# Kernel optimization log

Hardware: AMD Instinct MI355X
Metric: run time of the kernel (lower is better)

The kernel has to match this reference:

```python
import jax, jax.numpy as jnp
import numpy as np

D_H = 128
BATCH = 131072


def setup_inputs() -> dict:
    key = jax.random.key(0)
    k_h, k_x, k_w = jax.random.split(key, 3)
    h = jax.random.normal(k_h, (BATCH, D_H), dtype=jnp.float32)
    x = jax.random.normal(k_x, (BATCH, 3 * D_H), dtype=jnp.float32)
    # Dense kernel (d_h, 3*d_h); original uses zeros init, but random weights
    # give a meaningful correctness baseline.
    W = jax.random.normal(k_w, (D_H, 3 * D_H), dtype=jnp.float32) * 0.05
    return {"h": h, "x": x, "W": W}


def reference(h, x, W):
    d_h = h.shape[-1]
    # recurrent_proj(h): (B, d_h) @ (d_h, 3*d_h) -> (B, 3*d_h)
    recurrent_t = jnp.einsum("bd,de->be", h, W)
    # input pre-activation uses first d_h slice; gates use remaining 2*d_h
    input_t = jnp.tanh(x[:, :d_h] + recurrent_t[:, :d_h])
    gates_t = jax.nn.sigmoid(x[:, d_h:] + recurrent_t[:, d_h:])
    input_gate_t, output_gate_t = jnp.split(gates_t, 2, axis=-1)
    forget_gate_t = 1.0 - input_gate_t  # tied gates
    h_new = input_t * input_gate_t + h * forget_gate_t
    y = jnp.tanh(h_new) * output_gate_t
    return (h_new, y)
```

## Files before the change

### kernel.cpp

```cpp
#include <hip/hip_runtime.h>
#include <hip/hip_bf16.h>

#define BATCH 131072
#define DH 128
#define D3 384

typedef float   f32x4  __attribute__((ext_vector_type(4)));
typedef __bf16  bf16x8 __attribute__((ext_vector_type(8)));
typedef unsigned short u16x8 __attribute__((ext_vector_type(8)));

__device__ __forceinline__ unsigned short f2bf(float f) {
    unsigned u = __builtin_bit_cast(unsigned, f);
    u += 0x7fffu + ((u >> 16) & 1u);
    return (unsigned short)(u >> 16);
}

__device__ __forceinline__ float fast_tanh(float v) {
    float e = __expf(2.0f * v);
    return (e - 1.0f) * __builtin_amdgcn_rcpf(e + 1.0f);
}
__device__ __forceinline__ float fast_sigmoid(float z) {
    return __builtin_amdgcn_rcpf(1.0f + __expf(-z));
}

__global__ void prep_kernel(const float* __restrict__ W, unsigned short* __restrict__ wt) {
    int i   = blockIdx.x * 256 + threadIdx.x;
    int col = i >> 7;
    int k   = i & 127;
    wt[i] = f2bf(W[k * D3 + col]);
}

__global__ __launch_bounds__(256) void fused_kernel(
    const float* __restrict__ h, const float* __restrict__ x,
    const unsigned short* __restrict__ wt, float* __restrict__ out)
{
    const int wave = (blockIdx.x * 256 + (int)threadIdx.x) >> 6;
    const int lane = threadIdx.x & 63;
    const int c    = lane & 15;
    const int g    = lane >> 4;
    const int R    = wave * 16;

    bf16x8 a[4];
    {
        const float* hrow = h + (size_t)(R + c) * DH;
        #pragma unroll
        for (int s = 0; s < 4; ++s) {
            const float4* p = reinterpret_cast<const float4*>(hrow + 32 * s + 8 * g);
            float4 u0 = p[0], u1 = p[1];
            u16x8 t;
            t[0]=f2bf(u0.x); t[1]=f2bf(u0.y); t[2]=f2bf(u0.z); t[3]=f2bf(u0.w);
            t[4]=f2bf(u1.x); t[5]=f2bf(u1.y); t[6]=f2bf(u1.z); t[7]=f2bf(u1.w);
            a[s] = __builtin_bit_cast(bf16x8, t);
        }
    }

    f32x4 acc[24];
    #pragma unroll
    for (int i = 0; i < 24; ++i) acc[i] = (f32x4){0.f, 0.f, 0.f, 0.f};

    #pragma unroll
    for (int n = 0; n < 24; ++n) {
        const u16x8* wp = reinterpret_cast<const u16x8*>(wt + (16 * n + c) * DH);
        #pragma unroll
        for (int s = 0; s < 4; ++s) {
            u16x8 bv = wp[4 * s + g];
            acc[n] = __builtin_amdgcn_mfma_f32_16x16x32_bf16(
                a[s], __builtin_bit_cast(bf16x8, bv), acc[n], 0, 0, 0);
        }
    }

    const size_t ybase = (size_t)BATCH * DH;
    #pragma unroll
    for (int j = 0; j < 4; ++j) {
        const int row = R + 4 * g + j;
        const float* xr = x + (size_t)row * D3;
        const float* hr = h + (size_t)row * DH;
        float* o0 = out + (size_t)row * DH;
        float* o1 = out + ybase + (size_t)row * DH;
        #pragma unroll
        for (int n = 0; n < 8; ++n) {
            const int d = 16 * n + c;
            float r0 = acc[n][j];
            float r1 = acc[8 + n][j];
            float r2 = acc[16 + n][j];
            float hv = hr[d];
            float it = fast_tanh(xr[d] + r0);
            float ig = fast_sigmoid(xr[DH + d] + r1);
            float og = fast_sigmoid(xr[2 * DH + d] + r2);
            float hn = it * ig + hv * (1.0f - ig);
            o0[d] = hn;
            o1[d] = fast_tanh(hn) * og;
        }
    }
}

extern "C" void kernel_launch(void* const* d_in, const int* in_sizes, int n_in,
                              void* d_out, int out_size, void* d_ws, size_t ws_size,
                              hipStream_t stream) {
    const float* h = (const float*)d_in[0];
    const float* x = (const float*)d_in[1];
    const float* W = (const float*)d_in[2];
    float* out = (float*)d_out;
    unsigned short* wt = (unsigned short*)d_ws;

    prep_kernel<<<192, 256, 0, stream>>>(W, wt);
    fused_kernel<<<BATCH / 16 / 4, 256, 0, stream>>>(h, x, wt, out);
}
```

Baseline: 409.7 us.

## Transpose MFMA operands so accumulators hold contiguous row elements, vectorize epilogue I/O

Swaps the MFMA operand roles (W as A, h as B) so each lane's accumulator holds 4 contiguous output columns of one row. This allows x to be preloaded into the accumulators with 16-byte nontemporal loads and outputs to be written with 16-byte nontemporal stores, replacing the scalar strided epilogue accesses. Work is split so two waves share a 16-row tile, each covering half the columns, which doubles the grid and cuts accumulator registers from 24 to 12 vectors. In exchange, h is loaded and converted twice per tile, and the prep kernel's write pattern changes.

```diff
diff --git a/kernel.cpp b/kernel.cpp
--- a/kernel.cpp
+++ b/kernel.cpp
@@ -14,7 +14,6 @@
     u += 0x7fffu + ((u >> 16) & 1u);
     return (unsigned short)(u >> 16);
 }
-
 __device__ __forceinline__ float fast_tanh(float v) {
     float e = __expf(2.0f * v);
     return (e - 1.0f) * __builtin_amdgcn_rcpf(e + 1.0f);
@@ -24,10 +23,9 @@
 }
 
 __global__ void prep_kernel(const float* __restrict__ W, unsigned short* __restrict__ wt) {
-    int i   = blockIdx.x * 256 + threadIdx.x;
-    int col = i >> 7;
-    int k   = i & 127;
-    wt[i] = f2bf(W[k * D3 + col]);
+    const int k = blockIdx.x;
+    const int e = threadIdx.x;
+    wt[e * DH + k] = f2bf(W[k * D3 + e]);
 }
 
 __global__ __launch_bounds__(256) void fused_kernel(
@@ -38,59 +36,67 @@
     const int lane = threadIdx.x & 63;
     const int c    = lane & 15;
     const int g    = lane >> 4;
-    const int R    = wave * 16;
+    const int tile = wave >> 1;
+    const int q    = wave & 1;
+    const int row  = tile * 16 + c;
+    const int dbase = 64 * q + 4 * g;
 
-    bf16x8 a[4];
-    {
-        const float* hrow = h + (size_t)(R + c) * DH;
+    const float* xr = x + (size_t)row * D3;
+    const float* hr = h + (size_t)row * DH;
+
+    f32x4 acc[3][4];
+    #pragma unroll
+    for (int grp = 0; grp < 3; ++grp) {
         #pragma unroll
-        for (int s = 0; s < 4; ++s) {
-            const float4* p = reinterpret_cast<const float4*>(hrow + 32 * s + 8 * g);
-            float4 u0 = p[0], u1 = p[1];
-            u16x8 t;
-            t[0]=f2bf(u0.x); t[1]=f2bf(u0.y); t[2]=f2bf(u0.z); t[3]=f2bf(u0.w);
-            t[4]=f2bf(u1.x); t[5]=f2bf(u1.y); t[6]=f2bf(u1.z); t[7]=f2bf(u1.w);
-            a[s] = __builtin_bit_cast(bf16x8, t);
+        for (int n = 0; n < 4; ++n) {
+            const f32x4* p = reinterpret_cast<const f32x4*>(xr + grp * DH + dbase + 16 * n);
+            acc[grp][n] = __builtin_nontemporal_load(p);
         }
     }
 
-    f32x4 acc[24];
+    bf16x8 b[4];
     #pragma unroll
-    for (int i = 0; i < 24; ++i) acc[i] = (f32x4){0.f, 0.f, 0.f, 0.f};
+    for (int s = 0; s < 4; ++s) {
+        const float4* p = reinterpret_cast<const float4*>(hr + 32 * s + 8 * g);
+        float4 u0 = p[0], u1 = p[1];
+        u16x8 t;
+        t[0]=f2bf(u0.x); t[1]=f2bf(u0.y); t[2]=f2bf(u0.z); t[3]=f2bf(u0.w);
+        t[4]=f2bf(u1.x); t[5]=f2bf(u1.y); t[6]=f2bf(u1.z); t[7]=f2bf(u1.w);
+        b[s] = __builtin_bit_cast(bf16x8, t);
+    }
 
     #pragma unroll
-    for (int n = 0; n < 24; ++n) {
-        const u16x8* wp = reinterpret_cast<const u16x8*>(wt + (16 * n + c) * DH);
+    for (int grp = 0; grp < 3; ++grp) {
         #pragma unroll
-        for (int s = 0; s < 4; ++s) {
-            u16x8 bv = wp[4 * s + g];
-            acc[n] = __builtin_amdgcn_mfma_f32_16x16x32_bf16(
-                a[s], __builtin_bit_cast(bf16x8, bv), acc[n], 0, 0, 0);
+        for (int n = 0; n < 4; ++n) {
+            const int ebase = grp * DH + 64 * q + 16 * n;
+            const u16x8* wp = reinterpret_cast<const u16x8*>(wt + (size_t)(ebase + c) * DH);
+            #pragma unroll
+            for (int s = 0; s < 4; ++s) {
+                acc[grp][n] = __builtin_amdgcn_mfma_f32_16x16x32_bf16(
+                    __builtin_bit_cast(bf16x8, wp[4 * s + g]), b[s], acc[grp][n], 0, 0, 0);
+            }
         }
     }
 
-    const size_t ybase = (size_t)BATCH * DH;
+    float* o0 = out + (size_t)row * DH;
+    float* o1 = out + (size_t)BATCH * DH + (size_t)row * DH;
     #pragma unroll
-    for (int j = 0; j < 4; ++j) {
-        const int row = R + 4 * g + j;
-        const float* xr = x + (size_t)row * D3;
-        const float* hr = h + (size_t)row * DH;
-        float* o0 = out + (size_t)row * DH;
-        float* o1 = out + ybase + (size_t)row * DH;
+    for (int n = 0; n < 4; ++n) {
+        const int d = dbase + 16 * n;
+        f32x4 hv = *reinterpret_cast<const f32x4*>(hr + d);
+        f32x4 v0, v1;
         #pragma unroll
-        for (int n = 0; n < 8; ++n) {
-            const int d = 16 * n + c;
-            float r0 = acc[n][j];
-            float r1 = acc[8 + n][j];
-            float r2 = acc[16 + n][j];
-            float hv = hr[d];
-            float it = fast_tanh(xr[d] + r0);
-            float ig = fast_sigmoid(xr[DH + d] + r1);
-            float og = fast_sigmoid(xr[2 * DH + d] + r2);
-            float hn = it * ig + hv * (1.0f - ig);
-            o0[d] = hn;
-            o1[d] = fast_tanh(hn) * og;
+        for (int j = 0; j < 4; ++j) {
+            float it = fast_tanh(acc[0][n][j]);
+            float ig = fast_sigmoid(acc[1][n][j]);
+            float og = fast_sigmoid(acc[2][n][j]);
+            float hn = it * ig + hv[j] * (1.0f - ig);
+            v0[j] = hn;
+            v1[j] = fast_tanh(hn) * og;
         }
+        __builtin_nontemporal_store(v0, reinterpret_cast<f32x4*>(o0 + d));
+        __builtin_nontemporal_store(v1, reinterpret_cast<f32x4*>(o1 + d));
     }
 }
 
@@ -103,6 +109,6 @@
     float* out = (float*)d_out;
     unsigned short* wt = (unsigned short*)d_ws;
 
-    prep_kernel<<<192, 256, 0, stream>>>(W, wt);
-    fused_kernel<<<BATCH / 16 / 4, 256, 0, stream>>>(h, x, wt, out);
+    prep_kernel<<<DH, D3, 0, stream>>>(W, wt);
+    fused_kernel<<<BATCH / 16 * 2 / 4, 256, 0, stream>>>(h, x, wt, out);
 }
```

Result: slower. 442.5 us (+8.0%).
